# Optimization experiments

Hardware: AMD Instinct MI355X
Metric: run time of the kernel (lower is better)

## Reference

```python
import jax, jax.numpy as jnp
import numpy as np

# Config values (mirrors NanoConfig dca_* fields)
WINDOW_SIZE = 512
GLOBAL_TOKENS = 64
RANDOM_BLOCKS = 8


def setup_inputs() -> dict:
    key = jax.random.key(0)
    S = 8192
    # rand_scores replaces torch's per-row randperm: top-k indices of an iid
    # random matrix per row == sampling RANDOM_BLOCKS columns w/o replacement.
    rand_scores = jax.random.normal(key, (S, S), dtype=jnp.float32)
    return {"seq_len": S, "rand_scores": rand_scores}


def reference(seq_len, rand_scores):
    idx = jnp.arange(seq_len)
    window_radius = WINDOW_SIZE // 2
    # local banded window: |i - j| <= radius
    local_mask = jnp.abs(idx[None, :] - idx[:, None]) <= window_radius  # [S,S]
    # global tokens: first g rows and first g cols fully connected
    g = min(GLOBAL_TOKENS, seq_len)
    global_mask = (idx[None, :] < g) | (idx[:, None] < g)  # [S,S]
    # random connections: RANDOM_BLOCKS distinct random columns per row
    _, rand_idx = jax.lax.top_k(rand_scores, RANDOM_BLOCKS)  # [S, k]
    random_mask = jnp.zeros((seq_len, seq_len), dtype=bool).at[
        idx[:, None], rand_idx
    ].set(True)

    mask = local_mask | global_mask | random_mask  # [S,S] bool

    row_counts = mask.sum(axis=-1).astype(jnp.int32)  # [S]
    row_offsets = jnp.concatenate(
        [jnp.zeros(1, dtype=jnp.int32), jnp.cumsum(row_counts)]
    )  # [S+1]
    # data-dependent size: computed eagerly (matches torch .nonzero semantics)
    col_indices = jnp.nonzero(mask)[1].astype(jnp.int32)  # [total_connections]
    total_connections = col_indices.shape[0]
    sparsity = jnp.asarray(total_connections / max(seq_len * seq_len, 1), jnp.float32)
    return mask, row_offsets, col_indices, row_counts, sparsity
```

## Files before the change

### kernel.cpp

```cpp
#include <hip/hip_runtime.h>

#define SDIM 8192
#define RAD  256
#define GTOK 64
#define KSEL 8
#define CAP  768
#define SLOTS (CAP / 64)
#define THRESH 2.2f

typedef float f32x4 __attribute__((ext_vector_type(4)));

__global__ __launch_bounds__(256) void pass1_kernel(const float* __restrict__ scores,
                                                    int* __restrict__ rand_idx,
                                                    int* __restrict__ counts,
                                                    float* __restrict__ cnt_out,
                                                    float* __restrict__ mask_out) {
    __shared__ float cand_v[CAP];
    __shared__ int   cand_i[CAP];
    __shared__ int   top8[KSEL];
    __shared__ int   cnt;
    const int row  = blockIdx.x;
    const int t    = threadIdx.x;
    const int lane = t & 63;
    if (t == 0) cnt = 0;
    __syncthreads();

    const f32x4* rowp = reinterpret_cast<const f32x4*>(scores + (size_t)row * SDIM);
    f32x4 d[8];
#pragma unroll
    for (int k = 0; k < 8; k++) d[k] = rowp[t + k * 256];

    int wlo = row - RAD; if (wlo < 0) wlo = 0;
    int whi = row + RAD; if (whi > SDIM - 1) whi = SDIM - 1;
    const unsigned wspan = (unsigned)(whi - wlo);
    const bool full = row < GTOK;
    f32x4* mrow = reinterpret_cast<f32x4*>(mask_out + (size_t)row * SDIM);
#pragma unroll
    for (int k = 0; k < 8; k++) {
        int f4 = t + k * 256;
        int jb = f4 * 4;
        f32x4 o;
#pragma unroll
        for (int e = 0; e < 4; e++) {
            int j = jb + e;
            o[e] = (full || (j < GTOK) || ((unsigned)(j - wlo) <= wspan)) ? 1.0f : 0.0f;
        }
        __builtin_nontemporal_store(o, mrow + f4);
    }

#pragma unroll
    for (int k = 0; k < 8; k++) {
        int jb = (t + k * 256) * 4;
#pragma unroll
        for (int e = 0; e < 4; e++) {
            float val = d[k][e];
            bool pred = val > THRESH;
            unsigned long long m = __ballot(pred);
            if (m != 0ull) {
                int base = 0;
                if (lane == 0) base = atomicAdd(&cnt, __popcll(m));
                base = __shfl(base, 0);
                int off = __builtin_amdgcn_mbcnt_lo((unsigned)m, 0);
                off = __builtin_amdgcn_mbcnt_hi((unsigned)(m >> 32), off);
                int p = base + off;
                if (pred && p < CAP) { cand_v[p] = val; cand_i[p] = jb + e; }
            }
        }
    }
    __syncthreads();

    const int n = cnt;
    const bool bad = (n < KSEL || n > CAP);

    if (!bad) {
        if (t < 64) {
            float sv[SLOTS]; int si[SLOTS];
#pragma unroll
            for (int s = 0; s < SLOTS; s++) {
                int c = t + s * 64;
                if (c < n) { sv[s] = cand_v[c]; si[s] = cand_i[c]; }
                else       { sv[s] = -INFINITY; si[s] = 0x7fffffff; }
            }
            for (int round = 0; round < KSEL; round++) {
                float bv = -INFINITY; int bi = 0x7fffffff;
#pragma unroll
                for (int s = 0; s < SLOTS; s++) {
                    if (sv[s] > bv || (sv[s] == bv && si[s] < bi)) { bv = sv[s]; bi = si[s]; }
                }
#pragma unroll
                for (int s = 1; s < 64; s <<= 1) {
                    float ov = __shfl_xor(bv, s);
                    int   oi = __shfl_xor(bi, s);
                    if (ov > bv || (ov == bv && oi < bi)) { bv = ov; bi = oi; }
                }
                if (t == 0) top8[round] = bi;
#pragma unroll
                for (int s = 0; s < SLOTS; s++)
                    if (si[s] == bi) sv[s] = -INFINITY;
            }
        }
    } else {
        for (int round = 0; round < KSEL; round++) {
            float bv = -INFINITY; int bi = 0x7fffffff;
            for (int k = 0; k < 8; k++) {
                int f4 = t + k * 256;
                f32x4 dd = rowp[f4];
                int jb = f4 * 4;
                for (int e = 0; e < 4; e++) {
                    int j = jb + e;
                    bool used = false;
                    for (int q = 0; q < round; q++) used = used || (top8[q] == j);
                    if (!used && dd[e] > bv) { bv = dd[e]; bi = j; }
                }
            }
            cand_v[t] = bv; cand_i[t] = bi;
            __syncthreads();
            if (t < 64) {
                for (int c = t + 64; c < 256; c += 64) {
                    float vv = cand_v[c]; int ii = cand_i[c];
                    if (vv > bv || (vv == bv && ii < bi)) { bv = vv; bi = ii; }
                }
#pragma unroll
                for (int s = 32; s > 0; s >>= 1) {
                    float ov = __shfl_down(bv, s);
                    int   oi = __shfl_down(bi, s);
                    if (ov > bv || (ov == bv && oi < bi)) { bv = ov; bi = oi; }
                }
                if (t == 0) top8[round] = bi;
            }
            __syncthreads();
        }
    }
    __syncthreads();

    if (t < KSEL) {
        int r = top8[t];
        rand_idx[row * KSEL + t] = r;
        mask_out[(size_t)row * SDIM + r] = 1.0f;
    }
    if (t == 0) {
        int c;
        if (full) c = SDIM;
        else {
            c = (whi - wlo + 1) + (wlo < GTOK ? wlo : GTOK);
#pragma unroll
            for (int q = 0; q < KSEL; q++) {
                int r = top8[q];
                if (r >= GTOK && (r < wlo || r > whi)) c++;
            }
        }
        counts[row] = c;
        cnt_out[row] = (float)c;
    }
}

__global__ __launch_bounds__(64) void partial_kernel(const int* __restrict__ counts,
                                                     int* __restrict__ partials) {
    int acc = counts[blockIdx.x * 64 + threadIdx.x];
#pragma unroll
    for (int s = 32; s > 0; s >>= 1) acc += __shfl_down(acc, s);
    if (threadIdx.x == 0) partials[blockIdx.x] = acc;
}

__global__ __launch_bounds__(256) void col_kernel(const int* __restrict__ rand_idx,
                                                  const int* __restrict__ counts,
                                                  const int* __restrict__ partials,
                                                  float* __restrict__ off_out,
                                                  float* __restrict__ col_out,
                                                  float* __restrict__ sp_out) {
    __shared__ float stage[SDIM];
    __shared__ int s_off, s_total;
    const int row = blockIdx.x;
    const int t   = threadIdx.x;

    if (t < 64) {
        const int g = row >> 6;
        int acc = 0;
        for (int h = t; h < g; h += 64) acc += partials[h];
        for (int i = (g << 6) + t; i < row; i += 64) acc += counts[i];
#pragma unroll
        for (int s = 32; s > 0; s >>= 1) acc += __shfl_down(acc, s);
        if (t == 0) s_off = acc;
    }

    int r[KSEL];
#pragma unroll
    for (int q = 0; q < KSEL; q++) r[q] = rand_idx[row * KSEL + q];
    const bool full = row < GTOK;
    int wlo = row - RAD; if (wlo < 0) wlo = 0;
    int whi = row + RAD; if (whi > SDIM - 1) whi = SDIM - 1;

    const int jb = t * 32;
    unsigned int bm;
    int pos;
    if (full) {
        bm = ~0u;
        pos = jb;
    } else if (jb + 31 < GTOK) {
        bm = ~0u;
        pos = jb;
    } else {
        bm = 0u;
        int lo = wlo > jb ? wlo : jb;
        int hi = whi < jb + 31 ? whi : jb + 31;
        if (lo <= hi) {
            int a = lo - jb, z = hi - jb;
            unsigned hiM = (z == 31) ? ~0u : ((1u << (z + 1)) - 1u);
            unsigned loM = (1u << a) - 1u;
            bm = hiM & ~loM;
        }
#pragma unroll
        for (int q = 0; q < KSEL; q++)
            if ((r[q] >> 5) == t) bm |= 1u << (r[q] & 31);
        int glob   = jb < GTOK ? jb : GTOK;
        int bandlo = wlo > GTOK ? wlo : GTOK;
        int bandhi = jb < whi + 1 ? jb : whi + 1;
        int band   = bandhi - bandlo; if (band < 0) band = 0;
        int extr = 0;
#pragma unroll
        for (int q = 0; q < KSEL; q++) {
            int rq = r[q];
            bool ex = (rq >= GTOK) && (rq < wlo || rq > whi);
            extr += (ex && rq < jb) ? 1 : 0;
        }
        pos = glob + band + extr;
    }
    if (t == 255) s_total = pos + __popc(bm);

    for (int e = 0; e < 32; e++) {
        if ((bm >> e) & 1u) stage[pos++] = (float)(jb + e);
    }
    __syncthreads();
    const int offset = s_off;
    const int total  = s_total;
    for (int i = t; i < total; i += 256)
        __builtin_nontemporal_store(stage[i], col_out + offset + i);

    if (t == 0) {
        off_out[row] = (float)offset;
        if (row == SDIM - 1) {
            int tot = offset + total;
            off_out[SDIM] = (float)tot;
            sp_out[0] = (float)tot / 67108864.0f;
        }
    }
}

extern "C" void kernel_launch(void* const* d_in, const int* in_sizes, int n_in,
                              void* d_out, int out_size, void* d_ws, size_t ws_size,
                              hipStream_t stream) {
    const float* scores = (const float*)d_in[1];

    float* out_f    = (float*)d_out;
    float* mask_out = out_f;
    float* off_out  = out_f + (size_t)SDIM * SDIM;
    float* col_out  = off_out + (SDIM + 1);
    const long long TC = (long long)out_size
                       - ((long long)SDIM * SDIM + (SDIM + 1) + SDIM + 1);
    float* cnt_out = col_out + TC;
    float* sp_out  = cnt_out + SDIM;

    int* rand_idx = (int*)d_ws;
    int* counts   = rand_idx + SDIM * KSEL;
    int* partials = counts + SDIM;

    pass1_kernel<<<SDIM, 256, 0, stream>>>(scores, rand_idx, counts, cnt_out, mask_out);
    partial_kernel<<<SDIM / 64, 64, 0, stream>>>(counts, partials);
    col_kernel<<<SDIM, 256, 0, stream>>>(rand_idx, counts, partials,
                                         off_out, col_out, sp_out);
}
```

Baseline: 128.5 us.

## Split mask writing and top-k selection into separate blocks per row

Pass1 now launches two blocks per row. Even blocks write the dense local/global mask row, and odd blocks load scores and run the top-8 selection. The scatter of random-column ones into the mask moves to col_kernel, so it cannot race with the mask writer. Mask stores switch from nontemporal to regular stores, and the per-element predicate is skipped for chunks outside the band. The aim is more parallelism and overlap of the write-heavy and read-heavy work, at the cost of extra blocks and an ordering dependency that now lives in a later kernel.

```diff
diff --git a/kernel.cpp b/kernel.cpp
--- a/kernel.cpp
+++ b/kernel.cpp
@@ -19,34 +19,48 @@
     __shared__ int   cand_i[CAP];
     __shared__ int   top8[KSEL];
     __shared__ int   cnt;
-    const int row  = blockIdx.x;
+    const int bid  = blockIdx.x;
+    const int row  = bid >> 1;
     const int t    = threadIdx.x;
     const int lane = t & 63;
-    if (t == 0) cnt = 0;
-    __syncthreads();
-
-    const f32x4* rowp = reinterpret_cast<const f32x4*>(scores + (size_t)row * SDIM);
-    f32x4 d[8];
-#pragma unroll
-    for (int k = 0; k < 8; k++) d[k] = rowp[t + k * 256];
 
     int wlo = row - RAD; if (wlo < 0) wlo = 0;
     int whi = row + RAD; if (whi > SDIM - 1) whi = SDIM - 1;
     const unsigned wspan = (unsigned)(whi - wlo);
     const bool full = row < GTOK;
-    f32x4* mrow = reinterpret_cast<f32x4*>(mask_out + (size_t)row * SDIM);
-#pragma unroll
-    for (int k = 0; k < 8; k++) {
-        int f4 = t + k * 256;
-        int jb = f4 * 4;
-        f32x4 o;
-#pragma unroll
-        for (int e = 0; e < 4; e++) {
-            int j = jb + e;
-            o[e] = (full || (j < GTOK) || ((unsigned)(j - wlo) <= wspan)) ? 1.0f : 0.0f;
-        }
-        __builtin_nontemporal_store(o, mrow + f4);
-    }
+
+    if ((bid & 1) == 0) {
+        f32x4* mrow = reinterpret_cast<f32x4*>(mask_out + (size_t)row * SDIM);
+        if (full) {
+            const f32x4 ones = {1.0f, 1.0f, 1.0f, 1.0f};
+#pragma unroll
+            for (int k = 0; k < 8; k++) mrow[t + k * 256] = ones;
+        } else {
+#pragma unroll
+            for (int k = 0; k < 8; k++) {
+                int f4 = t + k * 256;
+                int jb = f4 * 4;
+                f32x4 o = {0.0f, 0.0f, 0.0f, 0.0f};
+                if ((jb < GTOK) || (jb + 3 >= wlo && jb <= whi)) {
+#pragma unroll
+                    for (int e = 0; e < 4; e++) {
+                        int j = jb + e;
+                        o[e] = ((j < GTOK) || ((unsigned)(j - wlo) <= wspan)) ? 1.0f : 0.0f;
+                    }
+                }
+                mrow[f4] = o;
+            }
+        }
+        return;
+    }
+
+    if (t == 0) cnt = 0;
+    __syncthreads();
+
+    const f32x4* rowp = reinterpret_cast<const f32x4*>(scores + (size_t)row * SDIM);
+    f32x4 d[8];
+#pragma unroll
+    for (int k = 0; k < 8; k++) d[k] = rowp[t + k * 256];
 
 #pragma unroll
     for (int k = 0; k < 8; k++) {
@@ -133,11 +147,7 @@
     }
     __syncthreads();
 
-    if (t < KSEL) {
-        int r = top8[t];
-        rand_idx[row * KSEL + t] = r;
-        mask_out[(size_t)row * SDIM + r] = 1.0f;
-    }
+    if (t < KSEL) rand_idx[row * KSEL + t] = top8[t];
     if (t == 0) {
         int c;
         if (full) c = SDIM;
@@ -167,7 +177,8 @@
                                                   const int* __restrict__ partials,
                                                   float* __restrict__ off_out,
                                                   float* __restrict__ col_out,
-                                                  float* __restrict__ sp_out) {
+                                                  float* __restrict__ sp_out,
+                                                  float* __restrict__ mask_out) {
     __shared__ float stage[SDIM];
     __shared__ int s_off, s_total;
     const int row = blockIdx.x;
@@ -183,6 +194,11 @@
         if (t == 0) s_off = acc;
     }
 
+    if (t < KSEL) {
+        int r = rand_idx[row * KSEL + t];
+        mask_out[(size_t)row * SDIM + r] = 1.0f;
+    }
+
     int r[KSEL];
 #pragma unroll
     for (int q = 0; q < KSEL; q++) r[q] = rand_idx[row * KSEL + q];
@@ -193,10 +209,7 @@
     const int jb = t * 32;
     unsigned int bm;
     int pos;
-    if (full) {
-        bm = ~0u;
-        pos = jb;
-    } else if (jb + 31 < GTOK) {
+    if (full || jb + 31 < GTOK) {
         bm = ~0u;
         pos = jb;
     } else {
@@ -264,8 +277,8 @@
     int* counts   = rand_idx + SDIM * KSEL;
     int* partials = counts + SDIM;
 
-    pass1_kernel<<<SDIM, 256, 0, stream>>>(scores, rand_idx, counts, cnt_out, mask_out);
+    pass1_kernel<<<SDIM * 2, 256, 0, stream>>>(scores, rand_idx, counts, cnt_out, mask_out);
     partial_kernel<<<SDIM / 64, 64, 0, stream>>>(counts, partials);
     col_kernel<<<SDIM, 256, 0, stream>>>(rand_idx, counts, partials,
-                                         off_out, col_out, sp_out);
-}
+                                         off_out, col_out, sp_out, mask_out);
+}
```

After: 162.2 us. +26.2%, slower.

## Process one row per wavefront in pass1 to remove block barriers

Applied to the files above, without the earlier changes.

Remaps the selection kernel so each 64-lane wave handles a whole row (four rows per block), keeping top-8 results in registers and using wave shuffles instead of block-wide barriers. Mask stores become regular stores with a cheaper range check that skips out-of-window chunks, and the candidate capacity is reduced. This aims to cut synchronization and idle threads, but each wave now streams its row in a serial chunk loop and loses the nontemporal store hint.

```diff
diff --git a/kernel.cpp b/kernel.cpp
--- a/kernel.cpp
+++ b/kernel.cpp
@@ -4,7 +4,7 @@
 #define RAD  256
 #define GTOK 64
 #define KSEL 8
-#define CAP  768
+#define CAP  512
 #define SLOTS (CAP / 64)
 #define THRESH 2.2f
 
@@ -15,137 +15,138 @@
                                                     int* __restrict__ counts,
                                                     float* __restrict__ cnt_out,
                                                     float* __restrict__ mask_out) {
-    __shared__ float cand_v[CAP];
-    __shared__ int   cand_i[CAP];
-    __shared__ int   top8[KSEL];
-    __shared__ int   cnt;
-    const int row  = blockIdx.x;
+    __shared__ float cand_v[4][CAP];
+    __shared__ int   cand_i[4][CAP];
+    __shared__ int   cnt[4];
     const int t    = threadIdx.x;
+    const int w    = t >> 6;
     const int lane = t & 63;
-    if (t == 0) cnt = 0;
-    __syncthreads();
-
-    const f32x4* rowp = reinterpret_cast<const f32x4*>(scores + (size_t)row * SDIM);
-    f32x4 d[8];
-#pragma unroll
-    for (int k = 0; k < 8; k++) d[k] = rowp[t + k * 256];
+    const int row  = blockIdx.x * 4 + w;
+    if (lane == 0) cnt[w] = 0;
 
     int wlo = row - RAD; if (wlo < 0) wlo = 0;
     int whi = row + RAD; if (whi > SDIM - 1) whi = SDIM - 1;
     const unsigned wspan = (unsigned)(whi - wlo);
     const bool full = row < GTOK;
+
+    const f32x4* rowp = reinterpret_cast<const f32x4*>(scores + (size_t)row * SDIM);
     f32x4* mrow = reinterpret_cast<f32x4*>(mask_out + (size_t)row * SDIM);
-#pragma unroll
-    for (int k = 0; k < 8; k++) {
-        int f4 = t + k * 256;
-        int jb = f4 * 4;
-        f32x4 o;
-#pragma unroll
-        for (int e = 0; e < 4; e++) {
-            int j = jb + e;
-            o[e] = (full || (j < GTOK) || ((unsigned)(j - wlo) <= wspan)) ? 1.0f : 0.0f;
-        }
-        __builtin_nontemporal_store(o, mrow + f4);
-    }
-
-#pragma unroll
-    for (int k = 0; k < 8; k++) {
-        int jb = (t + k * 256) * 4;
-#pragma unroll
-        for (int e = 0; e < 4; e++) {
-            float val = d[k][e];
-            bool pred = val > THRESH;
-            unsigned long long m = __ballot(pred);
-            if (m != 0ull) {
-                int base = 0;
-                if (lane == 0) base = atomicAdd(&cnt, __popcll(m));
-                base = __shfl(base, 0);
-                int off = __builtin_amdgcn_mbcnt_lo((unsigned)m, 0);
-                off = __builtin_amdgcn_mbcnt_hi((unsigned)(m >> 32), off);
-                int p = base + off;
-                if (pred && p < CAP) { cand_v[p] = val; cand_i[p] = jb + e; }
-            }
-        }
-    }
-    __syncthreads();
-
-    const int n = cnt;
+
+    for (int c = 0; c < 4; c++) {
+        const int cb = c * 512;
+        f32x4 d[8];
+#pragma unroll
+        for (int k = 0; k < 8; k++) d[k] = rowp[cb + k * 64 + lane];
+
+#pragma unroll
+        for (int k = 0; k < 8; k++) {
+            int f4 = cb + k * 64 + lane;
+            int jb = f4 * 4;
+            f32x4 o = {0.0f, 0.0f, 0.0f, 0.0f};
+            if (full) {
+                o = {1.0f, 1.0f, 1.0f, 1.0f};
+            } else if ((jb < GTOK) || (jb + 3 >= wlo && jb <= whi)) {
+#pragma unroll
+                for (int e = 0; e < 4; e++) {
+                    int j = jb + e;
+                    o[e] = ((j < GTOK) || ((unsigned)(j - wlo) <= wspan)) ? 1.0f : 0.0f;
+                }
+            }
+            mrow[f4] = o;
+        }
+
+#pragma unroll
+        for (int k = 0; k < 8; k++) {
+            int jb = (cb + k * 64 + lane) * 4;
+#pragma unroll
+            for (int e = 0; e < 4; e++) {
+                float val = d[k][e];
+                bool pred = val > THRESH;
+                unsigned long long m = __ballot(pred);
+                if (m != 0ull) {
+                    int base = 0;
+                    if (lane == 0) base = atomicAdd(&cnt[w], __popcll(m));
+                    base = __shfl(base, 0);
+                    int off = __builtin_amdgcn_mbcnt_lo((unsigned)m, 0);
+                    off = __builtin_amdgcn_mbcnt_hi((unsigned)(m >> 32), off);
+                    int p = base + off;
+                    if (pred && p < CAP) { cand_v[w][p] = val; cand_i[w][p] = jb + e; }
+                }
+            }
+        }
+    }
+
+    const int n = cnt[w];
     const bool bad = (n < KSEL || n > CAP);
+    int top8r[KSEL];
 
     if (!bad) {
-        if (t < 64) {
-            float sv[SLOTS]; int si[SLOTS];
+        float sv[SLOTS]; int si[SLOTS];
+#pragma unroll
+        for (int s = 0; s < SLOTS; s++) {
+            int c = lane + s * 64;
+            if (c < n) { sv[s] = cand_v[w][c]; si[s] = cand_i[w][c]; }
+            else       { sv[s] = -INFINITY;    si[s] = 0x7fffffff;   }
+        }
+#pragma unroll
+        for (int round = 0; round < KSEL; round++) {
+            float bv = -INFINITY; int bi = 0x7fffffff;
 #pragma unroll
             for (int s = 0; s < SLOTS; s++) {
-                int c = t + s * 64;
-                if (c < n) { sv[s] = cand_v[c]; si[s] = cand_i[c]; }
-                else       { sv[s] = -INFINITY; si[s] = 0x7fffffff; }
-            }
-            for (int round = 0; round < KSEL; round++) {
-                float bv = -INFINITY; int bi = 0x7fffffff;
-#pragma unroll
-                for (int s = 0; s < SLOTS; s++) {
-                    if (sv[s] > bv || (sv[s] == bv && si[s] < bi)) { bv = sv[s]; bi = si[s]; }
-                }
-#pragma unroll
-                for (int s = 1; s < 64; s <<= 1) {
-                    float ov = __shfl_xor(bv, s);
-                    int   oi = __shfl_xor(bi, s);
-                    if (ov > bv || (ov == bv && oi < bi)) { bv = ov; bi = oi; }
-                }
-                if (t == 0) top8[round] = bi;
-#pragma unroll
-                for (int s = 0; s < SLOTS; s++)
-                    if (si[s] == bi) sv[s] = -INFINITY;
-            }
+                if (sv[s] > bv || (sv[s] == bv && si[s] < bi)) { bv = sv[s]; bi = si[s]; }
+            }
+#pragma unroll
+            for (int s = 1; s < 64; s <<= 1) {
+                float ov = __shfl_xor(bv, s);
+                int   oi = __shfl_xor(bi, s);
+                if (ov > bv || (ov == bv && oi < bi)) { bv = ov; bi = oi; }
+            }
+            top8r[round] = bi;
+#pragma unroll
+            for (int s = 0; s < SLOTS; s++)
+                if (si[s] == bi) sv[s] = -INFINITY;
         }
     } else {
         for (int round = 0; round < KSEL; round++) {
             float bv = -INFINITY; int bi = 0x7fffffff;
-            for (int k = 0; k < 8; k++) {
-                int f4 = t + k * 256;
-                f32x4 dd = rowp[f4];
-                int jb = f4 * 4;
-                for (int e = 0; e < 4; e++) {
-                    int j = jb + e;
-                    bool used = false;
-                    for (int q = 0; q < round; q++) used = used || (top8[q] == j);
-                    if (!used && dd[e] > bv) { bv = dd[e]; bi = j; }
+            for (int c = 0; c < 4; c++) {
+                const int cb = c * 512;
+#pragma unroll
+                for (int k = 0; k < 8; k++) {
+                    f32x4 dd = rowp[cb + k * 64 + lane];
+                    int jb = (cb + k * 64 + lane) * 4;
+#pragma unroll
+                    for (int e = 0; e < 4; e++) {
+                        int j = jb + e;
+                        bool used = false;
+                        for (int q = 0; q < round; q++) used = used || (top8r[q] == j);
+                        if (!used && dd[e] > bv) { bv = dd[e]; bi = j; }
+                    }
                 }
             }
-            cand_v[t] = bv; cand_i[t] = bi;
-            __syncthreads();
-            if (t < 64) {
-                for (int c = t + 64; c < 256; c += 64) {
-                    float vv = cand_v[c]; int ii = cand_i[c];
-                    if (vv > bv || (vv == bv && ii < bi)) { bv = vv; bi = ii; }
-                }
-#pragma unroll
-                for (int s = 32; s > 0; s >>= 1) {
-                    float ov = __shfl_down(bv, s);
-                    int   oi = __shfl_down(bi, s);
-                    if (ov > bv || (ov == bv && oi < bi)) { bv = ov; bi = oi; }
-                }
-                if (t == 0) top8[round] = bi;
-            }
-            __syncthreads();
-        }
-    }
-    __syncthreads();
-
-    if (t < KSEL) {
-        int r = top8[t];
-        rand_idx[row * KSEL + t] = r;
+#pragma unroll
+            for (int s = 1; s < 64; s <<= 1) {
+                float ov = __shfl_xor(bv, s);
+                int   oi = __shfl_xor(bi, s);
+                if (ov > bv || (ov == bv && oi < bi)) { bv = ov; bi = oi; }
+            }
+            top8r[round] = bi;
+        }
+    }
+
+    if (lane < KSEL) {
+        int r = top8r[lane];
+        rand_idx[row * KSEL + lane] = r;
         mask_out[(size_t)row * SDIM + r] = 1.0f;
     }
-    if (t == 0) {
+    if (lane == 0) {
         int c;
         if (full) c = SDIM;
         else {
             c = (whi - wlo + 1) + (wlo < GTOK ? wlo : GTOK);
 #pragma unroll
             for (int q = 0; q < KSEL; q++) {
-                int r = top8[q];
+                int r = top8r[q];
                 if (r >= GTOK && (r < wlo || r > whi)) c++;
             }
         }
@@ -193,10 +194,7 @@
     const int jb = t * 32;
     unsigned int bm;
     int pos;
-    if (full) {
-        bm = ~0u;
-        pos = jb;
-    } else if (jb + 31 < GTOK) {
+    if (full || jb + 31 < GTOK) {
         bm = ~0u;
         pos = jb;
     } else {
@@ -264,7 +262,7 @@
     int* counts   = rand_idx + SDIM * KSEL;
     int* partials = counts + SDIM;
 
-    pass1_kernel<<<SDIM, 256, 0, stream>>>(scores, rand_idx, counts, cnt_out, mask_out);
+    pass1_kernel<<<SDIM / 4, 256, 0, stream>>>(scores, rand_idx, counts, cnt_out, mask_out);
     partial_kernel<<<SDIM / 64, 64, 0, stream>>>(counts, partials);
     col_kernel<<<SDIM, 256, 0, stream>>>(rand_idx, counts, partials,
                                          off_out, col_out, sp_out);
```

Result: slower. 155.3 us (+20.8%).
